# Performance work log

Measured on AMD Instinct MI355X. Metric: run time of the kernel, lower is better.

The kernel has to match this reference:

```python
import jax, jax.numpy as jnp
import numpy as np

RATIO = 0.2  # init ratio


def setup_inputs() -> dict:
    key = jax.random.key(0)
    inputs = jax.random.normal(key, (8, 19, 512, 1024), dtype=jnp.float32)
    return {"inputs": inputs}


def reference(inputs):
    # inputs: (N, C, H, W) logits
    N, C, H, W = inputs.shape
    p = jax.nn.softmax(inputs, axis=1)          # applySoftMax=True
    argpred = jnp.argmax(p, axis=1)              # (N, H, W)

    def image_weight(ap):
        # histogram of predicted classes over C bins (histc with min=0, max=C-1)
        h = jnp.zeros((C,), jnp.float32).at[ap.reshape(-1)].add(1.0)
        h = jnp.where(h == 0.0, 1.0, h)          # hist[hist==0] = 1
        return (h.sum() / h) ** RATIO            # (C,)

    weights = jax.vmap(image_weight)(argpred)    # (N, C), detached in original
    weights = jax.lax.stop_gradient(weights)

    loss = -(p ** 2) * weights[:, :, None, None]  # (N, C, H, W)
    return loss.mean()                            # reduction='mean'
```

## Files before the change

### kernel.cpp

```cpp
#include <hip/hip_runtime.h>

#define N_IMG 8
#define C_CLS 19
#define H_DIM 512
#define W_DIM 1024
#define HW (H_DIM * W_DIM)
#define HW4 (HW / 4)
#define TOTAL_ELEMS (N_IMG * C_CLS * HW)
#define RATIO 0.2f

#define BLOCKS_X 256
#define BLOCK_THREADS 256
#define ITERS 2

__device__ __forceinline__ float& f4c(float4& v, int k) {
    return reinterpret_cast<float*>(&v)[k];
}

__global__ __launch_bounds__(BLOCK_THREADS) void iw_pass1(
    const float* __restrict__ in,
    float* __restrict__ Q,
    int* __restrict__ Hist)
{
    const int n = blockIdx.y;
    const float4* base4 = reinterpret_cast<const float4*>(in + (size_t)n * C_CLS * HW);

    float q[C_CLS];
    int   hc[C_CLS];
#pragma unroll
    for (int c = 0; c < C_CLS; ++c) { q[c] = 0.0f; hc[c] = 0; }

    const int tid = threadIdx.x;
    int i = blockIdx.x * BLOCK_THREADS + tid;

#pragma unroll 1
    for (int it = 0; it < ITERS; ++it, i += BLOCKS_X * BLOCK_THREADS) {
        float4 x4[C_CLS];
#pragma unroll
        for (int c = 0; c < C_CLS; ++c)
            x4[c] = base4[(size_t)c * HW4 + i];

#pragma unroll
        for (int k = 0; k < 4; ++k) {
            float m = f4c(x4[0], k);
            int   am = 0;
#pragma unroll
            for (int c = 1; c < C_CLS; ++c) {
                float xc = f4c(x4[c], k);
                if (xc > m) { m = xc; am = c; }
            }
            float S = 0.0f;
#pragma unroll
            for (int c = 0; c < C_CLS; ++c) {
                float e = __expf(f4c(x4[c], k) - m);
                S += e;
                f4c(x4[c], k) = e * e;
            }
            float inv = 1.0f / (S * S);
#pragma unroll
            for (int c = 0; c < C_CLS; ++c) {
                q[c] = fmaf(f4c(x4[c], k), inv, q[c]);
                hc[c] += (am == c) ? 1 : 0;
            }
        }
    }

#pragma unroll
    for (int c = 0; c < C_CLS; ++c) {
        float v  = q[c];
        int   hv = hc[c];
#pragma unroll
        for (int off = 32; off > 0; off >>= 1) {
            v  += __shfl_xor(v, off, 64);
            hv += __shfl_xor(hv, off, 64);
        }
        q[c] = v; hc[c] = hv;
    }

    __shared__ float qs[4 * C_CLS];
    __shared__ int   hs[4 * C_CLS];
    const int wave = tid >> 6, lane = tid & 63;
    if (lane == 0) {
#pragma unroll
        for (int c = 0; c < C_CLS; ++c) {
            qs[wave * C_CLS + c] = q[c];
            hs[wave * C_CLS + c] = hc[c];
        }
    }
    __syncthreads();
    if (tid < C_CLS) {
        float s  = qs[tid] + qs[C_CLS + tid] + qs[2 * C_CLS + tid] + qs[3 * C_CLS + tid];
        int   hv = hs[tid] + hs[C_CLS + tid] + hs[2 * C_CLS + tid] + hs[3 * C_CLS + tid];
        atomicAdd(&Q[n * C_CLS + tid], s);
        atomicAdd(&Hist[n * C_CLS + tid], hv);
    }
}

__global__ __launch_bounds__(64) void iw_pass2(
    const float* __restrict__ Q,
    const int* __restrict__ Hist,
    float* __restrict__ out)
{
    const int t = threadIdx.x;
    float loss = 0.0f;
    if (t < N_IMG) {
        float h[C_CLS];
        float hs = 0.0f;
#pragma unroll
        for (int c = 0; c < C_CLS; ++c) {
            float v = (float)Hist[t * C_CLS + c];
            v = (v == 0.0f) ? 1.0f : v;
            h[c] = v;
            hs += v;
        }
#pragma unroll
        for (int c = 0; c < C_CLS; ++c) {
            float w = powf(hs / h[c], RATIO);
            loss = fmaf(w, Q[t * C_CLS + c], loss);
        }
    }
    loss += __shfl_xor(loss, 1, 64);
    loss += __shfl_xor(loss, 2, 64);
    loss += __shfl_xor(loss, 4, 64);
    if (t == 0)
        out[0] = -loss / (float)TOTAL_ELEMS;
}

extern "C" void kernel_launch(void* const* d_in, const int* in_sizes, int n_in,
                              void* d_out, int out_size, void* d_ws, size_t ws_size,
                              hipStream_t stream)
{
    const float* in = (const float*)d_in[0];
    float* out = (float*)d_out;

    float* Q  = (float*)d_ws;
    int* Hist = (int*)((char*)d_ws + N_IMG * C_CLS * sizeof(float));

    hipMemsetAsync(d_ws, 0, N_IMG * C_CLS * (sizeof(float) + sizeof(int)), stream);

    dim3 grid(BLOCKS_X, N_IMG);
    iw_pass1<<<grid, BLOCK_THREADS, 0, stream>>>(in, Q, Hist);
    iw_pass2<<<1, 64, 0, stream>>>(Q, Hist, out);
}
```

Before: 432.9 us.

## Use wave ballot for argmax histogram, one tile per thread, double grid

Replaces the per-thread histogram counters and their shuffle reduction with wave-wide ballot plus popcount, so every lane holds the wave total. The grid-stride loop over two iterations is removed and the x-grid doubled, so each thread handles exactly one float4 tile per class. Launch bounds now request four blocks per CU to limit register use. This cuts shuffle work and adds parallelism, at the cost of twice as many blocks and twice as many atomics, and possible spills under the tighter register cap.

```diff
diff --git a/kernel.cpp b/kernel.cpp
--- a/kernel.cpp
+++ b/kernel.cpp
@@ -9,82 +9,79 @@
 #define TOTAL_ELEMS (N_IMG * C_CLS * HW)
 #define RATIO 0.2f
 
-#define BLOCKS_X 256
+#define BLOCKS_X 512
 #define BLOCK_THREADS 256
-#define ITERS 2
 
 __device__ __forceinline__ float& f4c(float4& v, int k) {
     return reinterpret_cast<float*>(&v)[k];
 }
 
-__global__ __launch_bounds__(BLOCK_THREADS) void iw_pass1(
+__global__ __launch_bounds__(BLOCK_THREADS, 4) void iw_pass1(
     const float* __restrict__ in,
     float* __restrict__ Q,
     int* __restrict__ Hist)
 {
     const int n = blockIdx.y;
     const float4* base4 = reinterpret_cast<const float4*>(in + (size_t)n * C_CLS * HW);
+    const int i = blockIdx.x * BLOCK_THREADS + threadIdx.x;
+
+    float4 x4[C_CLS];
+#pragma unroll
+    for (int c = 0; c < C_CLS; ++c)
+        x4[c] = base4[(size_t)c * HW4 + i];
 
     float q[C_CLS];
-    int   hc[C_CLS];
 #pragma unroll
-    for (int c = 0; c < C_CLS; ++c) { q[c] = 0.0f; hc[c] = 0; }
+    for (int c = 0; c < C_CLS; ++c) q[c] = 0.0f;
 
-    const int tid = threadIdx.x;
-    int i = blockIdx.x * BLOCK_THREADS + tid;
+    int hw_cnt[C_CLS];
+#pragma unroll
+    for (int c = 0; c < C_CLS; ++c) hw_cnt[c] = 0;
 
-#pragma unroll 1
-    for (int it = 0; it < ITERS; ++it, i += BLOCKS_X * BLOCK_THREADS) {
-        float4 x4[C_CLS];
+#pragma unroll
+    for (int k = 0; k < 4; ++k) {
+        float m = f4c(x4[0], k);
+        int   am = 0;
+#pragma unroll
+        for (int c = 1; c < C_CLS; ++c) {
+            float xc = f4c(x4[c], k);
+            if (xc > m) { m = xc; am = c; }
+        }
 #pragma unroll
         for (int c = 0; c < C_CLS; ++c)
-            x4[c] = base4[(size_t)c * HW4 + i];
+            hw_cnt[c] += (int)__popcll(__ballot(am == c));
 
+        float S = 0.0f;
 #pragma unroll
-        for (int k = 0; k < 4; ++k) {
-            float m = f4c(x4[0], k);
-            int   am = 0;
+        for (int c = 0; c < C_CLS; ++c) {
+            float e = __expf(f4c(x4[c], k) - m);
+            S += e;
+            f4c(x4[c], k) = e * e;
+        }
+        float inv = 1.0f / (S * S);
 #pragma unroll
-            for (int c = 1; c < C_CLS; ++c) {
-                float xc = f4c(x4[c], k);
-                if (xc > m) { m = xc; am = c; }
-            }
-            float S = 0.0f;
-#pragma unroll
-            for (int c = 0; c < C_CLS; ++c) {
-                float e = __expf(f4c(x4[c], k) - m);
-                S += e;
-                f4c(x4[c], k) = e * e;
-            }
-            float inv = 1.0f / (S * S);
-#pragma unroll
-            for (int c = 0; c < C_CLS; ++c) {
-                q[c] = fmaf(f4c(x4[c], k), inv, q[c]);
-                hc[c] += (am == c) ? 1 : 0;
-            }
-        }
+        for (int c = 0; c < C_CLS; ++c)
+            q[c] = fmaf(f4c(x4[c], k), inv, q[c]);
     }
 
 #pragma unroll
     for (int c = 0; c < C_CLS; ++c) {
-        float v  = q[c];
-        int   hv = hc[c];
+        float v = q[c];
 #pragma unroll
-        for (int off = 32; off > 0; off >>= 1) {
-            v  += __shfl_xor(v, off, 64);
-            hv += __shfl_xor(hv, off, 64);
-        }
-        q[c] = v; hc[c] = hv;
+        for (int off = 32; off > 0; off >>= 1)
+            v += __shfl_xor(v, off, 64);
+        q[c] = v;
     }
 
     __shared__ float qs[4 * C_CLS];
     __shared__ int   hs[4 * C_CLS];
+    const int tid = threadIdx.x;
     const int wave = tid >> 6, lane = tid & 63;
     if (lane == 0) {
 #pragma unroll
         for (int c = 0; c < C_CLS; ++c) {
             qs[wave * C_CLS + c] = q[c];
-            hs[wave * C_CLS + c] = hc[c];
+            hs[wave * C_CLS + c] = hw_cnt[c];
         }
     }
     __syncthreads();
```

Measured after the change: 422.1 us. -2.5%, faster.
